# Optimization experiments

Hardware: AMD Instinct MI355X
Metric: run time of the kernel (lower is better)

Reference implementation:

```python
import jax, jax.numpy as jnp
import numpy as np

N_HEADS = 16
N_KV_HEADS = 4
HEAD_DIM = 128
NEG_INF = -1e9


def setup_inputs() -> dict:
    key = jax.random.key(0)
    ks = jax.random.split(key, 6)
    bs, seq, d_model = 2, 2048, 2048
    x = jax.random.normal(ks[0], (bs, seq, d_model), jnp.float32)
    # RoPE table: theta = 10000^{-2i/head_dim}, angle = pos * theta
    inv_freq = 1.0 / (10000.0 ** (jnp.arange(0, HEAD_DIM, 2, dtype=jnp.float32) / HEAD_DIM))
    ang = jnp.arange(seq, dtype=jnp.float32)[:, None] * inv_freq[None, :]  # [seq, head_dim/2]
    freqs_cos = jnp.cos(ang)
    freqs_sin = jnp.sin(ang)
    # causal additive mask
    mask = jnp.where(jnp.tril(jnp.ones((seq, seq), dtype=bool)), 0.0, NEG_INF).astype(jnp.float32)
    s = 1.0 / np.sqrt(d_model)
    wq = jax.random.normal(ks[1], (d_model, N_HEADS * HEAD_DIM), jnp.float32) * s
    wk = jax.random.normal(ks[2], (d_model, N_KV_HEADS * HEAD_DIM), jnp.float32) * s
    wv = jax.random.normal(ks[3], (d_model, N_KV_HEADS * HEAD_DIM), jnp.float32) * s
    wo = jax.random.normal(ks[4], (N_HEADS * HEAD_DIM, d_model), jnp.float32) * s
    return {"x": x, "freqs_cos": freqs_cos, "freqs_sin": freqs_sin, "mask": mask,
            "wq": wq, "wk": wk, "wv": wv, "wo": wo}


def _rope(t, cos, sin):
    # t: [b, h, s, d]; cos/sin: [s, d/2]
    b, h, s, d = t.shape
    tp = t.reshape(b, h, s, d // 2, 2)
    x0, x1 = tp[..., 0], tp[..., 1]
    c = cos[None, None, :, :]
    sn = sin[None, None, :, :]
    o0 = x0 * c - x1 * sn
    o1 = x0 * sn + x1 * c
    return jnp.stack([o0, o1], axis=-1).reshape(b, h, s, d)


def reference(x, freqs_cos, freqs_sin, mask, wq, wk, wv, wo):
    bs, seq, d_model = x.shape
    rep = N_HEADS // N_KV_HEADS
    q = (x @ wq).reshape(bs, seq, N_HEADS, HEAD_DIM).transpose(0, 2, 1, 3)
    k = (x @ wk).reshape(bs, seq, N_KV_HEADS, HEAD_DIM).transpose(0, 2, 1, 3)
    v = (x @ wv).reshape(bs, seq, N_KV_HEADS, HEAD_DIM).transpose(0, 2, 1, 3)
    q = _rope(q, freqs_cos, freqs_sin)
    k = _rope(k, freqs_cos, freqs_sin)
    # GQA: group q heads over kv heads instead of materially repeating kv
    qg = q.reshape(bs, N_KV_HEADS, rep, seq, HEAD_DIM)
    scores = jnp.einsum('bgrsd,bgtd->bgrst', qg, k) / np.sqrt(HEAD_DIM)
    scores = scores + mask[None, None, None, :, :]
    attn = jax.nn.softmax(scores, axis=-1)
    out = jnp.einsum('bgrst,bgtd->bgrsd', attn, v)
    out = out.reshape(bs, N_HEADS, seq, HEAD_DIM).transpose(0, 2, 1, 3).reshape(bs, seq, -1)
    return out @ wo
```

## Files before the change

kernel.cpp:

```cpp
#include <hip/hip_runtime.h>
#include <hip/hip_bf16.h>

#define SEQ 2048
#define DM 2048
#define NH 16
#define NKV 4
#define HD 128

typedef float f32x4 __attribute__((ext_vector_type(4)));
typedef short s16x8 __attribute__((ext_vector_type(8)));
typedef short s16x4 __attribute__((ext_vector_type(4)));

__device__ inline __hip_bfloat16 f2b(float f) { return __float2bfloat16(f); }
__device__ inline float b2f_us(unsigned short u) { return __uint_as_float(((unsigned)u) << 16); }
__device__ inline short f2b_s(float f) {
    __hip_bfloat16 h = __float2bfloat16(f);
    return *(short*)&h;
}

__device__ inline void gl_lds16(const void* g, void* l) {
    __builtin_amdgcn_global_load_lds((const __attribute__((address_space(1))) void*)g,
                                     (__attribute__((address_space(3))) void*)l, 16, 0, 0);
}

__global__ void cast_kernel(const float* __restrict__ in, __hip_bfloat16* __restrict__ out, int n) {
    int i = (blockIdx.x * 256 + threadIdx.x) * 4;
    if (i < n) {
        float4 v = *(const float4*)(in + i);
        __hip_bfloat16 o4[4] = {f2b(v.x), f2b(v.y), f2b(v.z), f2b(v.w)};
        *(ushort4*)(out + i) = *(ushort4*)o4;
    }
}

__global__ void transpose_cast(const float* __restrict__ in, __hip_bfloat16* __restrict__ out,
                               int K, int N) {
    __shared__ float tile[32][33];
    int n0 = blockIdx.x * 32, k0 = blockIdx.y * 32;
    int tx = threadIdx.x, ty = threadIdx.y;
    for (int r = ty; r < 32; r += 8)
        tile[r][tx] = in[(size_t)(k0 + r) * N + n0 + tx];
    __syncthreads();
    for (int r = ty; r < 32; r += 8)
        out[(size_t)(n0 + r) * K + k0 + tx] = f2b(tile[tx][r]);
}

template <int OUT_F32>
__global__ __launch_bounds__(256, 3) void gemm_bt(
    const __hip_bfloat16* __restrict__ A,
    const __hip_bfloat16* __restrict__ Bt,
    void* __restrict__ Cp, int M, int N, int Kd) {
    __shared__ __hip_bfloat16 As[128 * 64];
    __shared__ __hip_bfloat16 Bs[128 * 64];
    const int nx = gridDim.x, ny = gridDim.y;
    const int pid = blockIdx.y * nx + blockIdx.x;
    const int GM = 8;
    const int grp = pid / (GM * nx);
    const int first = grp * GM;
    const int gsz = (ny - first < GM) ? (ny - first) : GM;
    const int mt = first + (pid % gsz);
    const int ntile = (pid % (GM * nx)) / gsz;
    const int m0 = mt * 128, n0 = ntile * 128;

    const int t = threadIdx.x;
    const int wv = t >> 6, lane = t & 63;
    const int wm = (wv >> 1) * 64, wn = (wv & 1) * 64;
    const int lrow = lane & 15, quad = lane >> 4;
    f32x4 acc[4][4];
    f32x4 z4 = {0.f, 0.f, 0.f, 0.f};
    for (int i = 0; i < 4; ++i)
        for (int j = 0; j < 4; ++j) acc[i][j] = z4;

    for (int k0 = 0; k0 < Kd; k0 += 64) {
        __syncthreads();
        for (int i = 0; i < 4; ++i) {
            int flat = i * 256 + t;
            int row = flat >> 3;
            int cb = (flat & 7) ^ (row & 7);
            gl_lds16(A + (size_t)(m0 + row) * Kd + k0 + cb * 8, &As[flat * 8]);
            gl_lds16(Bt + (size_t)(n0 + row) * Kd + k0 + cb * 8, &Bs[flat * 8]);
        }
        __syncthreads();
        for (int kk = 0; kk < 2; ++kk) {
            s16x8 af[4], bf[4];
            for (int i = 0; i < 4; ++i) {
                int ra = wm + i * 16 + lrow;
                int rb = wn + i * 16 + lrow;
                int pba = ((kk * 4 + quad) ^ (ra & 7)) * 8;
                int pbb = ((kk * 4 + quad) ^ (rb & 7)) * 8;
                af[i] = *(const s16x8*)&As[ra * 64 + pba];
                bf[i] = *(const s16x8*)&Bs[rb * 64 + pbb];
            }
            for (int i = 0; i < 4; ++i)
                for (int j = 0; j < 4; ++j)
                    acc[i][j] = __builtin_amdgcn_mfma_f32_16x16x32_bf16(af[i], bf[j],
                                                                        acc[i][j], 0, 0, 0);
        }
    }
    for (int i = 0; i < 4; ++i)
        for (int j = 0; j < 4; ++j)
            for (int r = 0; r < 4; ++r) {
                int m = m0 + wm + i * 16 + quad * 4 + r;
                int n = n0 + wn + j * 16 + lrow;
                if (OUT_F32)
                    ((float*)Cp)[(size_t)m * N + n] = acc[i][j][r];
                else
                    ((__hip_bfloat16*)Cp)[(size_t)m * N + n] = f2b(acc[i][j][r]);
            }
}

__global__ void rope_reshape(const __hip_bfloat16* __restrict__ qkv,
                             const float* __restrict__ fcos, const float* __restrict__ fsin,
                             __hip_bfloat16* __restrict__ q, __hip_bfloat16* __restrict__ k) {
    int tok = blockIdx.x;
    int b = tok >> 11, s = tok & 2047;
    const __hip_bfloat16* row = qkv + (size_t)tok * 3072;
    for (int it = threadIdx.x; it < 320; it += 256) {
        int col = it * 8;
        s16x8 v = *(const s16x8*)(row + col);
        int p0 = (col & 127) >> 1;
        f32x4 c4 = *(const f32x4*)(fcos + s * 64 + p0);
        f32x4 s4 = *(const f32x4*)(fsin + s * 64 + p0);
        short outv[8];
        for (int p = 0; p < 4; ++p) {
            float x0 = b2f_us((unsigned short)v[2 * p]);
            float x1 = b2f_us((unsigned short)v[2 * p + 1]);
            outv[2 * p] = f2b_s(x0 * c4[p] - x1 * s4[p]);
            outv[2 * p + 1] = f2b_s(x0 * s4[p] + x1 * c4[p]);
        }
        int d = col & 127;
        if (col < 2048) {
            int h = col >> 7;
            *(s16x8*)(q + ((size_t)((b * NH + h) * SEQ + s)) * HD + d) = *(s16x8*)outv;
        } else {
            int h = (col - 2048) >> 7;
            *(s16x8*)(k + ((size_t)((b * NKV + h) * SEQ + s)) * HD + d) = *(s16x8*)outv;
        }
    }
}

__global__ void vtrans(const __hip_bfloat16* __restrict__ qkv, __hip_bfloat16* __restrict__ vt) {
    __shared__ __hip_bfloat16 tile[128][136];
    int s0 = blockIdx.x * 128;
    int bh = blockIdx.y;
    int b = bh >> 2, kvh = bh & 3;
    int t = threadIdx.x;
    for (int i = 0; i < 8; ++i) {
        int flat = (i * 256 + t) * 8;
        int row = flat >> 7, col = flat & 127;
        *(s16x8*)&tile[row][col] =
            *(const s16x8*)(qkv + (size_t)(b * SEQ + s0 + row) * 3072 + 2560 + kvh * 128 + col);
    }
    __syncthreads();
    for (int i = 0; i < 8; ++i) {
        int dd = i * 16 + (t >> 4);
        int ss = (t & 15) * 8;
        __hip_bfloat16 tmp[8];
        for (int j = 0; j < 8; ++j) tmp[j] = tile[ss + j][dd];
        *(s16x8*)(vt + ((size_t)((b * NKV + kvh) * HD + dd)) * SEQ + s0 + ss) = *(s16x8*)tmp;
    }
}

__global__ __launch_bounds__(512, 4) void attn_kernel(
    const __hip_bfloat16* __restrict__ q, const __hip_bfloat16* __restrict__ k,
    const __hip_bfloat16* __restrict__ vt, __hip_bfloat16* __restrict__ o) {
    __shared__ __hip_bfloat16 Ks[2][64][136];
    __shared__ __hip_bfloat16 Vs[2][128][72];

    const int bh = blockIdx.y;
    const int bx = (bh < 16) ? (int)(gridDim.x - 1 - blockIdx.x) : (int)blockIdx.x;
    const int b = bh >> 4, h = bh & 15;
    const int kvh = h >> 2;
    const int t = threadIdx.x;
    const int w = t >> 6, lane = t & 63;
    const int lrow = lane & 15, quad = lane >> 4;
    const int q0 = bx * 128;
    const int qrow = q0 + w * 16 + lrow;
    const float scale = 0.08838834764831845f;

    const __hip_bfloat16* qp = q + ((size_t)((b * NH + h) * SEQ + qrow)) * HD;
    s16x8 qf[4];
    for (int ks = 0; ks < 4; ++ks) qf[ks] = *(const s16x8*)(qp + ks * 32 + quad * 8);

    float m_i = -1e30f, l_i = 0.f;
    f32x4 accO[8];
    f32x4 z4 = {0.f, 0.f, 0.f, 0.f};
    for (int d = 0; d < 8; ++d) accO[d] = z4;

    const __hip_bfloat16* kbase = k + ((size_t)(b * NKV + kvh) * SEQ) * HD;
    const __hip_bfloat16* vbase = vt + ((size_t)(b * NKV + kvh) * HD) * SEQ;

    s16x8 kr[2], vr[2];
    auto load_tile = [&](int kt) {
        for (int i = 0; i < 2; ++i) {
            int flat = (i * 512 + t) * 8;
            kr[i] = *(const s16x8*)(kbase + (size_t)(kt * 64 + (flat >> 7)) * HD + (flat & 127));
            vr[i] = *(const s16x8*)(vbase + (size_t)(flat >> 6) * SEQ + kt * 64 + (flat & 63));
        }
    };
    auto store_tile = [&](int bsel) {
        for (int i = 0; i < 2; ++i) {
            int flat = (i * 512 + t) * 8;
            *(s16x8*)&Ks[bsel][flat >> 7][flat & 127] = kr[i];
            int row = flat >> 6, k0 = flat & 63;
            int pb = ((k0 >> 5) << 5) | (((k0 >> 2) & 2) << 3) | (((k0 >> 4) & 1) << 2);
            s16x4 lo = {vr[i][0], vr[i][1], vr[i][2], vr[i][3]};
            s16x4 hi = {vr[i][4], vr[i][5], vr[i][6], vr[i][7]};
            *(s16x4*)&Vs[bsel][row][pb] = lo;
            *(s16x4*)&Vs[bsel][row][pb + 8] = hi;
        }
    };

    const int nkt = 2 * bx + 2;
    load_tile(0);
    store_tile(0);

    for (int kt = 0; kt < nkt; ++kt) {
        const int cur = kt & 1;
        bool more = (kt + 1) < nkt;
        __syncthreads();
        if (more) load_tile(kt + 1);
        bool wave_active = (kt * 64 <= q0 + w * 16 + 15);
        bool mtile = (kt >= 2 * bx);

        if (wave_active) {
            float sv[4][4];
            for (int nt = 0; nt < 4; ++nt) {
                f32x4 sacc = z4;
                for (int ks = 0; ks < 4; ++ks) {
                    s16x8 kf = *(const s16x8*)&Ks[cur][nt * 16 + lrow][ks * 32 + quad * 8];
                    sacc = __builtin_amdgcn_mfma_f32_16x16x32_bf16(kf, qf[ks], sacc, 0, 0, 0);
                }
                for (int r = 0; r < 4; ++r) {
                    int key = kt * 64 + nt * 16 + quad * 4 + r;
                    sv[nt][r] = (mtile && key > qrow) ? -1e30f : sacc[r] * scale;
                }
            }
            float mt2 = -1e30f;
            for (int nt = 0; nt < 4; ++nt)
                for (int r = 0; r < 4; ++r) mt2 = fmaxf(mt2, sv[nt][r]);
            mt2 = fmaxf(mt2, __shfl_xor(mt2, 16, 64));
            mt2 = fmaxf(mt2, __shfl_xor(mt2, 32, 64));
            float mn = fmaxf(m_i, mt2);
            float alpha = __expf(m_i - mn);
            m_i = mn;
            float rs = 0.f;
            s16x8 pf0, pf1;
#pragma unroll
            for (int j = 0; j < 8; ++j) {
                float p0 = __expf(sv[j >> 2][j & 3] - mn);
                float p1 = __expf(sv[2 + (j >> 2)][j & 3] - mn);
                rs += p0 + p1;
                pf0[j] = f2b_s(p0);
                pf1[j] = f2b_s(p1);
            }
            rs += __shfl_xor(rs, 16, 64);
            rs += __shfl_xor(rs, 32, 64);
            l_i = l_i * alpha + rs;
            for (int d = 0; d < 8; ++d)
                for (int r = 0; r < 4; ++r) accO[d][r] *= alpha;
            for (int dt = 0; dt < 8; ++dt) {
                s16x8 vf0 = *(const s16x8*)&Vs[cur][dt * 16 + lrow][quad * 8];
                s16x8 vf1 = *(const s16x8*)&Vs[cur][dt * 16 + lrow][32 + quad * 8];
                accO[dt] = __builtin_amdgcn_mfma_f32_16x16x32_bf16(vf0, pf0, accO[dt], 0, 0, 0);
                accO[dt] = __builtin_amdgcn_mfma_f32_16x16x32_bf16(vf1, pf1, accO[dt], 0, 0, 0);
            }
        }

        if (more) store_tile(1 - cur);
    }
    float inv = 1.0f / l_i;
    __hip_bfloat16* op = o + (size_t)(b * SEQ + qrow) * DM + h * HD;
    for (int dt = 0; dt < 8; ++dt) {
        short ov[4];
        for (int r = 0; r < 4; ++r) ov[r] = f2b_s(accO[dt][r] * inv);
        *(s16x4*)(op + dt * 16 + quad * 4) = *(s16x4*)ov;
    }
}

extern "C" void kernel_launch(void* const* d_in, const int* in_sizes, int n_in,
                              void* d_out, int out_size, void* d_ws, size_t ws_size,
                              hipStream_t stream) {
    (void)in_sizes; (void)n_in; (void)out_size; (void)ws_size;
    const float* x  = (const float*)d_in[0];
    const float* fc = (const float*)d_in[1];
    const float* fs = (const float*)d_in[2];
    const float* wq = (const float*)d_in[4];
    const float* wk = (const float*)d_in[5];
    const float* wv = (const float*)d_in[6];
    const float* wo = (const float*)d_in[7];

    __hip_bfloat16* xb    = (__hip_bfloat16*)d_ws;
    __hip_bfloat16* wqkvt = xb + (size_t)8388608;
    __hip_bfloat16* wot   = wqkvt + (size_t)6291456;
    __hip_bfloat16* qkv   = wot + (size_t)4194304;
    __hip_bfloat16* qb    = xb;
    __hip_bfloat16* kb    = wqkvt;
    __hip_bfloat16* vtb   = wqkvt + (size_t)2097152;
    __hip_bfloat16* attno = qkv;

    cast_kernel<<<8192, 256, 0, stream>>>(x, xb, 8388608);
    transpose_cast<<<dim3(64, 64), dim3(32, 8), 0, stream>>>(wq, wqkvt, 2048, 2048);
    transpose_cast<<<dim3(16, 64), dim3(32, 8), 0, stream>>>(wk, wqkvt + (size_t)2048 * 2048, 2048, 512);
    transpose_cast<<<dim3(16, 64), dim3(32, 8), 0, stream>>>(wv, wqkvt + (size_t)2560 * 2048, 2048, 512);
    transpose_cast<<<dim3(64, 64), dim3(32, 8), 0, stream>>>(wo, wot, 2048, 2048);
    gemm_bt<0><<<dim3(24, 32), 256, 0, stream>>>(xb, wqkvt, qkv, 4096, 3072, 2048);
    rope_reshape<<<4096, 256, 0, stream>>>(qkv, fc, fs, qb, kb);
    vtrans<<<dim3(16, 8), 256, 0, stream>>>(qkv, vtb);
    attn_kernel<<<dim3(16, 32), 512, 0, stream>>>(qb, kb, vtb, attno);
    gemm_bt<1><<<dim3(16, 32), 256, 0, stream>>>(attno, wot, d_out, 4096, 2048, 2048);
}
```

Measured before the change: 335.6 us.

## Restructure attention into 64-row blocks with swizzled single-buffer LDS and lazy rescale

Attention blocks now cover 64 query rows with 256 threads, doubling the grid. K and V use a single XOR-swizzled shared buffer with no padding, replacing the padded double buffer. Q is pre-scaled in the RoPE kernel by scale*log2(e) so softmax can use exp2f directly. The running max is only rescaled when it grows by more than 8, which skips most alpha multiplies. The causal-mask branch is limited to the diagonal tile, and per-wave inactivity checks are dropped. The trade-offs are an extra barrier per tile, less load/compute overlap from single buffering, and some bf16 precision risk from the lazy rescale bound.

```diff
diff --git a/kernel.cpp b/kernel.cpp
--- a/kernel.cpp
+++ b/kernel.cpp
@@ -108,6 +108,7 @@
             }
 }
 
+#define QSC 0.12751744f
 __global__ void rope_reshape(const __hip_bfloat16* __restrict__ qkv,
                              const float* __restrict__ fcos, const float* __restrict__ fsin,
                              __hip_bfloat16* __restrict__ q, __hip_bfloat16* __restrict__ k) {
@@ -120,12 +121,13 @@
         int p0 = (col & 127) >> 1;
         f32x4 c4 = *(const f32x4*)(fcos + s * 64 + p0);
         f32x4 s4 = *(const f32x4*)(fsin + s * 64 + p0);
+        float scl = (col < 2048) ? QSC : 1.0f;
         short outv[8];
         for (int p = 0; p < 4; ++p) {
             float x0 = b2f_us((unsigned short)v[2 * p]);
             float x1 = b2f_us((unsigned short)v[2 * p + 1]);
-            outv[2 * p] = f2b_s(x0 * c4[p] - x1 * s4[p]);
-            outv[2 * p + 1] = f2b_s(x0 * s4[p] + x1 * c4[p]);
+            outv[2 * p] = f2b_s((x0 * c4[p] - x1 * s4[p]) * scl);
+            outv[2 * p + 1] = f2b_s((x0 * s4[p] + x1 * c4[p]) * scl);
         }
         int d = col & 127;
         if (col < 2048) {
@@ -160,22 +162,22 @@
     }
 }
 
-__global__ __launch_bounds__(512, 4) void attn_kernel(
+__global__ __launch_bounds__(256, 4) void attn_kernel(
     const __hip_bfloat16* __restrict__ q, const __hip_bfloat16* __restrict__ k,
     const __hip_bfloat16* __restrict__ vt, __hip_bfloat16* __restrict__ o) {
-    __shared__ __hip_bfloat16 Ks[2][64][136];
-    __shared__ __hip_bfloat16 Vs[2][128][72];
+    __shared__ __hip_bfloat16 Ks[64 * 128];
+    __shared__ __hip_bfloat16 Vs[128 * 64];
 
     const int bh = blockIdx.y;
-    const int bx = (bh < 16) ? (int)(gridDim.x - 1 - blockIdx.x) : (int)blockIdx.x;
+    const int flip = (blockIdx.y >> 3) & 1;
+    const int bx = flip ? (31 - (int)blockIdx.x) : (int)blockIdx.x;
     const int b = bh >> 4, h = bh & 15;
     const int kvh = h >> 2;
     const int t = threadIdx.x;
     const int w = t >> 6, lane = t & 63;
     const int lrow = lane & 15, quad = lane >> 4;
-    const int q0 = bx * 128;
+    const int q0 = bx * 64;
     const int qrow = q0 + w * 16 + lrow;
-    const float scale = 0.08838834764831845f;
 
     const __hip_bfloat16* qp = q + ((size_t)((b * NH + h) * SEQ + qrow)) * HD;
     s16x8 qf[4];
@@ -189,84 +191,92 @@
     const __hip_bfloat16* kbase = k + ((size_t)(b * NKV + kvh) * SEQ) * HD;
     const __hip_bfloat16* vbase = vt + ((size_t)(b * NKV + kvh) * HD) * SEQ;
 
-    s16x8 kr[2], vr[2];
+    s16x8 kr[4], vr[4];
     auto load_tile = [&](int kt) {
-        for (int i = 0; i < 2; ++i) {
-            int flat = (i * 512 + t) * 8;
+        for (int i = 0; i < 4; ++i) {
+            int flat = (i * 256 + t) * 8;
             kr[i] = *(const s16x8*)(kbase + (size_t)(kt * 64 + (flat >> 7)) * HD + (flat & 127));
             vr[i] = *(const s16x8*)(vbase + (size_t)(flat >> 6) * SEQ + kt * 64 + (flat & 63));
         }
     };
-    auto store_tile = [&](int bsel) {
-        for (int i = 0; i < 2; ++i) {
-            int flat = (i * 512 + t) * 8;
-            *(s16x8*)&Ks[bsel][flat >> 7][flat & 127] = kr[i];
-            int row = flat >> 6, k0 = flat & 63;
+    auto store_tile = [&]() {
+        for (int i = 0; i < 4; ++i) {
+            int flat = (i * 256 + t) * 8;
+            int krow = flat >> 7, kcol = flat & 127;
+            *(s16x8*)&Ks[krow * 128 + (((kcol >> 3) ^ (krow & 7)) << 3)] = kr[i];
+            int vrow = flat >> 6, k0 = flat & 63;
             int pb = ((k0 >> 5) << 5) | (((k0 >> 2) & 2) << 3) | (((k0 >> 4) & 1) << 2);
+            int blo = pb >> 3, sub = pb & 7;
             s16x4 lo = {vr[i][0], vr[i][1], vr[i][2], vr[i][3]};
             s16x4 hi = {vr[i][4], vr[i][5], vr[i][6], vr[i][7]};
-            *(s16x4*)&Vs[bsel][row][pb] = lo;
-            *(s16x4*)&Vs[bsel][row][pb + 8] = hi;
+            *(s16x4*)&Vs[vrow * 64 + ((blo ^ (vrow & 7)) << 3) + sub] = lo;
+            *(s16x4*)&Vs[vrow * 64 + (((blo + 1) ^ (vrow & 7)) << 3) + sub] = hi;
         }
     };
 
-    const int nkt = 2 * bx + 2;
+    const int nkt = bx + 1;
     load_tile(0);
-    store_tile(0);
+    store_tile();
 
     for (int kt = 0; kt < nkt; ++kt) {
-        const int cur = kt & 1;
-        bool more = (kt + 1) < nkt;
         __syncthreads();
+        const bool more = (kt + 1) < nkt;
         if (more) load_tile(kt + 1);
-        bool wave_active = (kt * 64 <= q0 + w * 16 + 15);
-        bool mtile = (kt >= 2 * bx);
-
-        if (wave_active) {
-            float sv[4][4];
-            for (int nt = 0; nt < 4; ++nt) {
-                f32x4 sacc = z4;
-                for (int ks = 0; ks < 4; ++ks) {
-                    s16x8 kf = *(const s16x8*)&Ks[cur][nt * 16 + lrow][ks * 32 + quad * 8];
-                    sacc = __builtin_amdgcn_mfma_f32_16x16x32_bf16(kf, qf[ks], sacc, 0, 0, 0);
-                }
+        const bool dia = (kt == bx);
+
+        float sv[4][4];
+        for (int nt = 0; nt < 4; ++nt) {
+            f32x4 sacc = z4;
+            const int row = nt * 16 + lrow;
+            for (int ks = 0; ks < 4; ++ks) {
+                s16x8 kf = *(const s16x8*)&Ks[row * 128 + (((ks * 4 + quad) ^ (lrow & 7)) << 3)];
+                sacc = __builtin_amdgcn_mfma_f32_16x16x32_bf16(kf, qf[ks], sacc, 0, 0, 0);
+            }
+            if (dia) {
                 for (int r = 0; r < 4; ++r) {
                     int key = kt * 64 + nt * 16 + quad * 4 + r;
-                    sv[nt][r] = (mtile && key > qrow) ? -1e30f : sacc[r] * scale;
+                    sv[nt][r] = (key > qrow) ? -1e30f : sacc[r];
                 }
+            } else {
+                for (int r = 0; r < 4; ++r) sv[nt][r] = sacc[r];
             }
-            float mt2 = -1e30f;
-            for (int nt = 0; nt < 4; ++nt)
-                for (int r = 0; r < 4; ++r) mt2 = fmaxf(mt2, sv[nt][r]);
-            mt2 = fmaxf(mt2, __shfl_xor(mt2, 16, 64));
-            mt2 = fmaxf(mt2, __shfl_xor(mt2, 32, 64));
+        }
+        float mt2 = -1e30f;
+        for (int nt = 0; nt < 4; ++nt)
+            for (int r = 0; r < 4; ++r) mt2 = fmaxf(mt2, sv[nt][r]);
+        mt2 = fmaxf(mt2, __shfl_xor(mt2, 16, 64));
+        mt2 = fmaxf(mt2, __shfl_xor(mt2, 32, 64));
+        if (!__all(mt2 <= m_i + 8.f)) {
             float mn = fmaxf(m_i, mt2);
-            float alpha = __expf(m_i - mn);
-            m_i = mn;
-            float rs = 0.f;
-            s16x8 pf0, pf1;
-#pragma unroll
-            for (int j = 0; j < 8; ++j) {
-                float p0 = __expf(sv[j >> 2][j & 3] - mn);
-                float p1 = __expf(sv[2 + (j >> 2)][j & 3] - mn);
-                rs += p0 + p1;
-                pf0[j] = f2b_s(p0);
-                pf1[j] = f2b_s(p1);
-            }
-            rs += __shfl_xor(rs, 16, 64);
-            rs += __shfl_xor(rs, 32, 64);
-            l_i = l_i * alpha + rs;
+            float alpha = exp2f(m_i - mn);
+            l_i *= alpha;
             for (int d = 0; d < 8; ++d)
                 for (int r = 0; r < 4; ++r) accO[d][r] *= alpha;
-            for (int dt = 0; dt < 8; ++dt) {
-                s16x8 vf0 = *(const s16x8*)&Vs[cur][dt * 16 + lrow][quad * 8];
-                s16x8 vf1 = *(const s16x8*)&Vs[cur][dt * 16 + lrow][32 + quad * 8];
-                accO[dt] = __builtin_amdgcn_mfma_f32_16x16x32_bf16(vf0, pf0, accO[dt], 0, 0, 0);
-                accO[dt] = __builtin_amdgcn_mfma_f32_16x16x32_bf16(vf1, pf1, accO[dt], 0, 0, 0);
-            }
-        }
-
-        if (more) store_tile(1 - cur);
+            m_i = mn;
+        }
+        float rs = 0.f;
+        s16x8 pf0, pf1;
+#pragma unroll
+        for (int j = 0; j < 8; ++j) {
+            float p0 = exp2f(sv[j >> 2][j & 3] - m_i);
+            float p1 = exp2f(sv[2 + (j >> 2)][j & 3] - m_i);
+            rs += p0 + p1;
+            pf0[j] = f2b_s(p0);
+            pf1[j] = f2b_s(p1);
+        }
+        rs += __shfl_xor(rs, 16, 64);
+        rs += __shfl_xor(rs, 32, 64);
+        l_i += rs;
+        for (int dt = 0; dt < 8; ++dt) {
+            const int vrow = dt * 16 + lrow;
+            s16x8 vf0 = *(const s16x8*)&Vs[vrow * 64 + ((quad ^ (lrow & 7)) << 3)];
+            s16x8 vf1 = *(const s16x8*)&Vs[vrow * 64 + (((4 + quad) ^ (lrow & 7)) << 3)];
+            accO[dt] = __builtin_amdgcn_mfma_f32_16x16x32_bf16(vf0, pf0, accO[dt], 0, 0, 0);
+            accO[dt] = __builtin_amdgcn_mfma_f32_16x16x32_bf16(vf1, pf1, accO[dt], 0, 0, 0);
+        }
+
+        __syncthreads();
+        if (more) store_tile();
     }
     float inv = 1.0f / l_i;
     __hip_bfloat16* op = o + (size_t)(b * SEQ + qrow) * DM + h * HD;
@@ -306,6 +316,6 @@
     gemm_bt<0><<<dim3(24, 32), 256, 0, stream>>>(xb, wqkvt, qkv, 4096, 3072, 2048);
     rope_reshape<<<4096, 256, 0, stream>>>(qkv, fc, fs, qb, kb);
     vtrans<<<dim3(16, 8), 256, 0, stream>>>(qkv, vtb);
-    attn_kernel<<<dim3(16, 32), 512, 0, stream>>>(qb, kb, vtb, attno);
+    attn_kernel<<<dim3(32, 32), 256, 0, stream>>>(qb, kb, vtb, attno);
     gemm_bt<1><<<dim3(16, 32), 256, 0, stream>>>(attno, wot, d_out, 4096, 2048, 2048);
 }
```

After: 380.8 us. +13.5%, slower.

## Fold softmax scale and log2e into Q, use exp2 with lazy rescaling

Applied to the files above, without the earlier changes.

The softmax scale times log2(e) is folded into Q during the RoPE pass, so the attention loop uses exp2 on the raw scores with no per-element multiply. The output rescale is skipped unless the running max grows by more than a threshold (FA4-style lazy rescaling). The mask select now runs only on diagonal tiles, and s_setprio raises wave priority around the MFMA sections. This trims VALU work in the softmax inner loop. In exchange, Q is rounded to bf16 after scaling, and p values can grow to 2^8 before renormalising, which could affect precision slightly.

```diff
diff --git a/kernel.cpp b/kernel.cpp
--- a/kernel.cpp
+++ b/kernel.cpp
@@ -108,6 +108,7 @@
             }
 }
 
+#define QSC 0.12751744f
 __global__ void rope_reshape(const __hip_bfloat16* __restrict__ qkv,
                              const float* __restrict__ fcos, const float* __restrict__ fsin,
                              __hip_bfloat16* __restrict__ q, __hip_bfloat16* __restrict__ k) {
@@ -120,12 +121,13 @@
         int p0 = (col & 127) >> 1;
         f32x4 c4 = *(const f32x4*)(fcos + s * 64 + p0);
         f32x4 s4 = *(const f32x4*)(fsin + s * 64 + p0);
+        float scl = (col < 2048) ? QSC : 1.0f;
         short outv[8];
         for (int p = 0; p < 4; ++p) {
             float x0 = b2f_us((unsigned short)v[2 * p]);
             float x1 = b2f_us((unsigned short)v[2 * p + 1]);
-            outv[2 * p] = f2b_s(x0 * c4[p] - x1 * s4[p]);
-            outv[2 * p + 1] = f2b_s(x0 * s4[p] + x1 * c4[p]);
+            outv[2 * p] = f2b_s((x0 * c4[p] - x1 * s4[p]) * scl);
+            outv[2 * p + 1] = f2b_s((x0 * s4[p] + x1 * c4[p]) * scl);
         }
         int d = col & 127;
         if (col < 2048) {
@@ -175,7 +177,6 @@
     const int lrow = lane & 15, quad = lane >> 4;
     const int q0 = bx * 128;
     const int qrow = q0 + w * 16 + lrow;
-    const float scale = 0.08838834764831845f;
 
     const __hip_bfloat16* qp = q + ((size_t)((b * NH + h) * SEQ + qrow)) * HD;
     s16x8 qf[4];
@@ -224,46 +225,59 @@
 
         if (wave_active) {
             float sv[4][4];
+            __builtin_amdgcn_s_setprio(1);
             for (int nt = 0; nt < 4; ++nt) {
                 f32x4 sacc = z4;
                 for (int ks = 0; ks < 4; ++ks) {
                     s16x8 kf = *(const s16x8*)&Ks[cur][nt * 16 + lrow][ks * 32 + quad * 8];
                     sacc = __builtin_amdgcn_mfma_f32_16x16x32_bf16(kf, qf[ks], sacc, 0, 0, 0);
                 }
-                for (int r = 0; r < 4; ++r) {
-                    int key = kt * 64 + nt * 16 + quad * 4 + r;
-                    sv[nt][r] = (mtile && key > qrow) ? -1e30f : sacc[r] * scale;
+                if (mtile) {
+                    for (int r = 0; r < 4; ++r) {
+                        int key = kt * 64 + nt * 16 + quad * 4 + r;
+                        sv[nt][r] = (key > qrow) ? -1e30f : sacc[r];
+                    }
+                } else {
+                    for (int r = 0; r < 4; ++r) sv[nt][r] = sacc[r];
                 }
             }
-            float mt2 = -1e30f;
-            for (int nt = 0; nt < 4; ++nt)
-                for (int r = 0; r < 4; ++r) mt2 = fmaxf(mt2, sv[nt][r]);
+            __builtin_amdgcn_s_setprio(0);
+            float mt2 = fmaxf(fmaxf(fmaxf(sv[0][0], sv[0][1]), fmaxf(sv[0][2], sv[0][3])),
+                              fmaxf(fmaxf(sv[1][0], sv[1][1]), fmaxf(sv[1][2], sv[1][3])));
+            mt2 = fmaxf(mt2,
+                        fmaxf(fmaxf(fmaxf(sv[2][0], sv[2][1]), fmaxf(sv[2][2], sv[2][3])),
+                              fmaxf(fmaxf(sv[3][0], sv[3][1]), fmaxf(sv[3][2], sv[3][3]))));
             mt2 = fmaxf(mt2, __shfl_xor(mt2, 16, 64));
             mt2 = fmaxf(mt2, __shfl_xor(mt2, 32, 64));
-            float mn = fmaxf(m_i, mt2);
-            float alpha = __expf(m_i - mn);
-            m_i = mn;
+            if (!__all(mt2 <= m_i + 8.f)) {
+                float mn = fmaxf(m_i, mt2);
+                float alpha = exp2f(m_i - mn);
+                l_i *= alpha;
+                for (int d = 0; d < 8; ++d)
+                    for (int r = 0; r < 4; ++r) accO[d][r] *= alpha;
+                m_i = mn;
+            }
             float rs = 0.f;
             s16x8 pf0, pf1;
 #pragma unroll
             for (int j = 0; j < 8; ++j) {
-                float p0 = __expf(sv[j >> 2][j & 3] - mn);
-                float p1 = __expf(sv[2 + (j >> 2)][j & 3] - mn);
+                float p0 = exp2f(sv[j >> 2][j & 3] - m_i);
+                float p1 = exp2f(sv[2 + (j >> 2)][j & 3] - m_i);
                 rs += p0 + p1;
                 pf0[j] = f2b_s(p0);
                 pf1[j] = f2b_s(p1);
             }
             rs += __shfl_xor(rs, 16, 64);
             rs += __shfl_xor(rs, 32, 64);
-            l_i = l_i * alpha + rs;
-            for (int d = 0; d < 8; ++d)
-                for (int r = 0; r < 4; ++r) accO[d][r] *= alpha;
+            l_i += rs;
+            __builtin_amdgcn_s_setprio(1);
             for (int dt = 0; dt < 8; ++dt) {
                 s16x8 vf0 = *(const s16x8*)&Vs[cur][dt * 16 + lrow][quad * 8];
                 s16x8 vf1 = *(const s16x8*)&Vs[cur][dt * 16 + lrow][32 + quad * 8];
                 accO[dt] = __builtin_amdgcn_mfma_f32_16x16x32_bf16(vf0, pf0, accO[dt], 0, 0, 0);
                 accO[dt] = __builtin_amdgcn_mfma_f32_16x16x32_bf16(vf1, pf1, accO[dt], 0, 0, 0);
             }
+            __builtin_amdgcn_s_setprio(0);
         }
 
         if (more) store_tile(1 - cur);
```

After: 322.1 us, median of 2. 1.04x faster.
